# Performance work log

Hardware: AMD Instinct MI355X
Metric: run time of the kernel (lower is better)

The kernel has to match this reference:

```python
import jax, jax.numpy as jnp
import numpy as np

D_INSTR, D_ACT, D_OBJ, TOK = 768, 7, 256, 256


def setup_inputs() -> dict:
    key = jax.random.key(0)
    ks = jax.random.split(key, 10)
    B, NDEMO, NOBJ = 256, 16, 64
    inp = {
        "instr_embedding": jax.random.normal(ks[0], (B, D_INSTR), jnp.float32),
        "demo_object_embeddings": jax.random.normal(ks[1], (NDEMO, B, NOBJ, D_OBJ), jnp.float32),
        "demo_actions": jax.random.normal(ks[2], (NDEMO, B, D_ACT), jnp.float32),
        "current_object_embeddings": jax.random.normal(ks[3], (B, NOBJ, D_OBJ), jnp.float32),
        # learned params (stored as (in, out); equivalent math to torch Linear)
        "W_instr": jax.random.normal(ks[4], (D_INSTR, TOK), jnp.float32) / np.sqrt(D_INSTR),
        "b_instr": jax.random.normal(ks[5], (TOK,), jnp.float32) * 0.01,
        "W_act": jax.random.normal(ks[6], (D_ACT, TOK), jnp.float32) / np.sqrt(D_ACT),
        "b_act": jax.random.normal(ks[7], (TOK,), jnp.float32) * 0.01,
        "W_obj": jax.random.normal(ks[8], (D_OBJ, TOK), jnp.float32) / np.sqrt(D_OBJ),
        "b_obj": jax.random.normal(ks[9], (TOK,), jnp.float32) * 0.01,
    }
    return inp


def reference(instr_embedding, demo_object_embeddings, demo_actions,
              current_object_embeddings, W_instr, b_instr, W_act, b_act,
              W_obj, b_obj):
    # Project everything in single batched GEMMs (structure is uniform across batch,
    # so the per-example Python loop in the original collapses to dense ops).
    instr_tok = instr_embedding @ W_instr + b_instr            # (B, T)
    demo_obj_tok = jnp.einsum('dbnf,ft->dbnt', demo_object_embeddings, W_obj) + b_obj  # (D,B,No,T)
    act_tok = jnp.einsum('dbf,ft->dbt', demo_actions, W_act) + b_act                   # (D,B,T)
    cur_tok = jnp.einsum('bnf,ft->bnt', current_object_embeddings, W_obj) + b_obj      # (B,No,T)

    D, B, No, T = demo_obj_tok.shape
    # Per demo: [objects..., action] -> (D, B, No+1, T), then interleave demos in order.
    demo_block = jnp.concatenate([demo_obj_tok, act_tok[:, :, None, :]], axis=2)
    demo_block = demo_block.transpose(1, 0, 2, 3).reshape(B, D * (No + 1), T)
    # Final sequence: [instr, demo1_objs, demo1_action, ..., current_objs]
    return jnp.concatenate([instr_tok[:, None, :], demo_block, cur_tok], axis=1)
```

## Files before the change

kernel.cpp:

```cpp
#include <hip/hip_runtime.h>
#include <hip/hip_bf16.h>
#include <stdint.h>

#define TOK   256
#define NOBJ  64
#define NDEMO 16
#define BATCH 256
#define SEQ   1105
#define NDG   (NDEMO * BATCH)
#define NGRP  (NDG + BATCH)
#define NHT   (NGRP * 2)
#define NG    4
#define OBJ_BLKS   (NHT / NG)
#define ACT_BLKS   512
#define INSTR_BLKS 128
#define TOTAL_BLKS (ACT_BLKS + INSTR_BLKS + OBJ_BLKS)

typedef __bf16 bf16x8 __attribute__((ext_vector_type(8)));
typedef float  f32x4  __attribute__((ext_vector_type(4)));

static __device__ __forceinline__ unsigned pack_bf16x2(float a, float b) {
    unsigned ua = __float_as_uint(a);
    unsigned ub = __float_as_uint(b);
    unsigned ra = (ua + 0x7FFFu + ((ua >> 16) & 1u)) >> 16;
    unsigned rb = (ub + 0x7FFFu + ((ub >> 16) & 1u)) >> 16;
    return (ra & 0xFFFFu) | (rb << 16);
}

static __device__ __forceinline__ uint16_t f32_to_bf16_bits(float a) {
    unsigned ua = __float_as_uint(a);
    return (uint16_t)((ua + 0x7FFFu + ((ua >> 16) & 1u)) >> 16);
}

static __device__ __forceinline__ bf16x8 pack8(float4 lo, float4 hi) {
    union { uint4 u; bf16x8 b; } r;
    r.u.x = pack_bf16x2(lo.x, lo.y);
    r.u.y = pack_bf16x2(lo.z, lo.w);
    r.u.z = pack_bf16x2(hi.x, hi.y);
    r.u.w = pack_bf16x2(hi.z, hi.w);
    return r.b;
}

static __device__ __forceinline__ void gload_lds16(const float* g, void* l) {
    __builtin_amdgcn_global_load_lds(
        (const __attribute__((address_space(1))) uint32_t*)g,
        (__attribute__((address_space(3))) uint32_t*)l,
        16, 0, 0);
}

__global__ void wconv_frag_kernel(const float* __restrict__ W, uint16_t* __restrict__ Wf) {
    int q = blockIdx.x * 256 + threadIdx.x;
    int lane = q & 63;
    int s  = (q >> 6) & 7;
    int j  = (q >> 9) & 3;
    int wc = (q >> 11) & 3;
    int tcol = wc * 64 + j * 16 + (lane & 15);
    int k0   = s * 32 + (lane >> 4) * 8;
    uint4 w;
    unsigned p[4];
#pragma unroll
    for (int h = 0; h < 4; ++h) {
        float a = W[(size_t)(k0 + 2 * h)     * TOK + tcol];
        float b = W[(size_t)(k0 + 2 * h + 1) * TOK + tcol];
        p[h] = pack_bf16x2(a, b);
    }
    w.x = p[0]; w.y = p[1]; w.z = p[2]; w.w = p[3];
    *reinterpret_cast<uint4*>(Wf + (size_t)q * 8) = w;
}

__global__ __launch_bounds__(256, 2) void fused_kernel(
    const float* __restrict__ demo_obj,
    const float* __restrict__ cur,
    const float* __restrict__ b_obj,
    const __bf16* __restrict__ Wf,
    const float* __restrict__ demo_act,
    const float* __restrict__ W_act,
    const float* __restrict__ b_act,
    const float* __restrict__ instr,
    const float* __restrict__ W_instr,
    const float* __restrict__ b_instr,
    float* __restrict__ out)
{
    __shared__ __align__(16) float lds[2 * 32 * TOK];
    int blk = blockIdx.x;
    int tid = threadIdx.x;

    if (blk >= ACT_BLKS + INSTR_BLKS) {
        int ob = blk - (ACT_BLKS + INSTR_BLKS);
        int h0 = ob * NG;
        const float* base = (h0 < 2 * NDG)
            ? demo_obj + (size_t)h0 * (32 * TOK)
            : cur + (size_t)(h0 - 2 * NDG) * (32 * TOK);

        int wave = tid >> 6, lane = tid & 63;
        int l15 = lane & 15, l4 = lane >> 4;
        int n0 = wave * 64;

        int sr = tid >> 6;
        int sc = tid & 63;
        auto STAGE = [&](int it, int bsel) {
            const float* sb = base + (size_t)it * (32 * TOK);
            float* dst = lds + bsel * (32 * TOK);
#pragma unroll
            for (int i = 0; i < 8; ++i) {
                int r = i * 4 + sr;
                int gch = r * 64 + (sc ^ (r & 7));
                gload_lds16(sb + (size_t)gch * 4, dst + (size_t)(i * 256 + tid) * 4);
            }
        };

        STAGE(0, 0);

        bf16x8 bf[4][8];
        {
            const __bf16* fb = Wf + ((size_t)wave * 32 * 64 + lane) * 8;
#pragma unroll
            for (int j = 0; j < 4; ++j)
#pragma unroll
                for (int s = 0; s < 8; ++s)
                    bf[j][s] = *reinterpret_cast<const bf16x8*>(fb + (size_t)(j * 8 + s) * 64 * 8);
        }

        float bv[4];
#pragma unroll
        for (int j = 0; j < 4; ++j) bv[j] = b_obj[n0 + j * 16 + l15];

#pragma unroll 1
        for (int it = 0; it < NG; ++it) {
            if (it + 1 < NG) {
                STAGE(it + 1, (it + 1) & 1);
                asm volatile("s_waitcnt vmcnt(8)" ::: "memory");
            } else {
                asm volatile("s_waitcnt vmcnt(0)" ::: "memory");
            }
            __builtin_amdgcn_s_barrier();
            __builtin_amdgcn_sched_barrier(0);

            const float* buf = lds + (it & 1) * (32 * TOK);

            f32x4 acc[2][4];
#pragma unroll
            for (int i = 0; i < 2; ++i)
#pragma unroll
                for (int j = 0; j < 4; ++j) {
                    f32x4 z = {0.0f, 0.0f, 0.0f, 0.0f};
                    acc[i][j] = z;
                }

#pragma unroll
            for (int s = 0; s < 8; ++s) {
                bf16x8 a[2];
#pragma unroll
                for (int i = 0; i < 2; ++i) {
                    int r = i * 16 + l15;
                    int c0 = s * 8 + l4 * 2;
                    float4 lo = *reinterpret_cast<const float4*>(buf + r * TOK + ((c0 ^ (r & 7)) * 4));
                    float4 hi = *reinterpret_cast<const float4*>(buf + r * TOK + (((c0 + 1) ^ (r & 7)) * 4));
                    a[i] = pack8(lo, hi);
                }
#pragma unroll
                for (int j = 0; j < 4; ++j) {
                    acc[0][j] = __builtin_amdgcn_mfma_f32_16x16x32_bf16(a[0], bf[j][s], acc[0][j], 0, 0, 0);
                    acc[1][j] = __builtin_amdgcn_mfma_f32_16x16x32_bf16(a[1], bf[j][s], acc[1][j], 0, 0, 0);
                }
            }

            int h = h0 + it;
            int g = h >> 1, half = h & 1;
            int row_base;
            if (h < 2 * NDG) {
                int d = g >> 8, b = g & 255;
                row_base = b * SEQ + 1 + d * (NOBJ + 1) + half * 32;
            } else {
                int b = g - NDG;
                row_base = b * SEQ + 1 + NDEMO * (NOBJ + 1) + half * 32;
            }
#pragma unroll
            for (int i = 0; i < 2; ++i)
#pragma unroll
                for (int j = 0; j < 4; ++j) {
                    int col = n0 + j * 16 + l15;
#pragma unroll
                    for (int r = 0; r < 4; ++r) {
                        int row = row_base + i * 16 + l4 * 4 + r;
                        out[(size_t)row * TOK + col] = acc[i][j][r] + bv[j];
                    }
                }

            __builtin_amdgcn_s_barrier();
        }

    } else if (blk < ACT_BLKS) {
        int g8 = blk * 8;
        int t = tid;
        float v[8];
        float bb = b_act[t];
#pragma unroll
        for (int r = 0; r < 8; ++r) v[r] = bb;
#pragma unroll
        for (int k = 0; k < 7; ++k) {
            float wv = W_act[k * TOK + t];
#pragma unroll
            for (int r = 0; r < 8; ++r)
                v[r] += demo_act[(size_t)(g8 + r) * 7 + k] * wv;
        }
#pragma unroll
        for (int r = 0; r < 8; ++r) {
            int g = g8 + r;
            int d = g >> 8, b = g & 255;
            out[(size_t)(b * SEQ + (d + 1) * (NOBJ + 1)) * TOK + t] = v[r];
        }

    } else {
        int b0 = (blk - ACT_BLKS) * 2;
        int t = tid;
        float* buf = lds;
        const float* src = instr + (size_t)b0 * 768;
#pragma unroll
        for (int i = 0; i < 6; ++i) buf[i * 256 + t] = src[i * 256 + t];
        __syncthreads();
        float a0 = b_instr[t], a1 = a0;
#pragma unroll 4
        for (int k = 0; k < 768; ++k) {
            float wv = W_instr[(size_t)k * TOK + t];
            a0 += buf[k] * wv;
            a1 += buf[768 + k] * wv;
        }
        out[(size_t)b0 * SEQ * TOK + t] = a0;
        out[(size_t)(b0 + 1) * SEQ * TOK + t] = a1;
    }
}

extern "C" void kernel_launch(void* const* d_in, const int* in_sizes, int n_in,
                              void* d_out, int out_size, void* d_ws, size_t ws_size,
                              hipStream_t stream) {
    (void)in_sizes; (void)n_in; (void)out_size; (void)ws_size;
    const float* instr    = (const float*)d_in[0];
    const float* demo_obj = (const float*)d_in[1];
    const float* demo_act = (const float*)d_in[2];
    const float* cur      = (const float*)d_in[3];
    const float* W_instr  = (const float*)d_in[4];
    const float* b_instr  = (const float*)d_in[5];
    const float* W_act    = (const float*)d_in[6];
    const float* b_act    = (const float*)d_in[7];
    const float* W_obj    = (const float*)d_in[8];
    const float* b_obj    = (const float*)d_in[9];
    float* out = (float*)d_out;

    uint16_t* Wf = (uint16_t*)d_ws;

    wconv_frag_kernel<<<32, 256, 0, stream>>>(W_obj, Wf);
    fused_kernel<<<TOTAL_BLKS, 256, 0, stream>>>(
        demo_obj, cur, b_obj, (const __bf16*)d_ws,
        demo_act, W_act, b_act, instr, W_instr, b_instr, out);
}
```

Before: 152.1 us.

## Switch object GEMM to 16-row tiles with triple-buffered LDS prefetch

Each object-projection step now covers 16 rows instead of 32, and each block processes 8 tiles. The LDS pipeline moves from double to triple buffering with a prefetch distance of two, and the barrier at the end of each iteration is dropped. LDS per block shrinks, which lets launch bounds ask for 3 blocks per SM. The aim is to overlap more of the global load latency with compute, at the cost of fewer MFMAs per LDS load and more complex vmcnt bookkeeping.

```diff
diff --git a/kernel.cpp b/kernel.cpp
--- a/kernel.cpp
+++ b/kernel.cpp
@@ -9,9 +9,9 @@
 #define SEQ   1105
 #define NDG   (NDEMO * BATCH)
 #define NGRP  (NDG + BATCH)
-#define NHT   (NGRP * 2)
-#define NG    4
-#define OBJ_BLKS   (NHT / NG)
+#define NQT   (NGRP * 4)
+#define NG    8
+#define OBJ_BLKS   (NQT / NG)
 #define ACT_BLKS   512
 #define INSTR_BLKS 128
 #define TOTAL_BLKS (ACT_BLKS + INSTR_BLKS + OBJ_BLKS)
@@ -68,7 +68,7 @@
     *reinterpret_cast<uint4*>(Wf + (size_t)q * 8) = w;
 }
 
-__global__ __launch_bounds__(256, 2) void fused_kernel(
+__global__ __launch_bounds__(256, 3) void fused_kernel(
     const float* __restrict__ demo_obj,
     const float* __restrict__ cur,
     const float* __restrict__ b_obj,
@@ -81,35 +81,31 @@
     const float* __restrict__ b_instr,
     float* __restrict__ out)
 {
-    __shared__ __align__(16) float lds[2 * 32 * TOK];
+    __shared__ __align__(16) float lds[3 * 16 * TOK];
     int blk = blockIdx.x;
     int tid = threadIdx.x;
 
     if (blk >= ACT_BLKS + INSTR_BLKS) {
         int ob = blk - (ACT_BLKS + INSTR_BLKS);
         int h0 = ob * NG;
-        const float* base = (h0 < 2 * NDG)
-            ? demo_obj + (size_t)h0 * (32 * TOK)
-            : cur + (size_t)(h0 - 2 * NDG) * (32 * TOK);
+        const float* base = (h0 < 4 * NDG)
+            ? demo_obj + (size_t)h0 * (16 * TOK)
+            : cur + (size_t)(h0 - 4 * NDG) * (16 * TOK);
 
         int wave = tid >> 6, lane = tid & 63;
         int l15 = lane & 15, l4 = lane >> 4;
         int n0 = wave * 64;
 
-        int sr = tid >> 6;
-        int sc = tid & 63;
         auto STAGE = [&](int it, int bsel) {
-            const float* sb = base + (size_t)it * (32 * TOK);
-            float* dst = lds + bsel * (32 * TOK);
-#pragma unroll
-            for (int i = 0; i < 8; ++i) {
-                int r = i * 4 + sr;
-                int gch = r * 64 + (sc ^ (r & 7));
+            const float* sb = base + (size_t)it * (16 * TOK);
+            float* dst = lds + bsel * (16 * TOK);
+#pragma unroll
+            for (int i = 0; i < 4; ++i) {
+                int r = i * 4 + wave;
+                int gch = r * 64 + (lane ^ (r & 7));
                 gload_lds16(sb + (size_t)gch * 4, dst + (size_t)(i * 256 + tid) * 4);
             }
         };
-
-        STAGE(0, 0);
 
         bf16x8 bf[4][8];
         {
@@ -120,74 +116,74 @@
                 for (int s = 0; s < 8; ++s)
                     bf[j][s] = *reinterpret_cast<const bf16x8*>(fb + (size_t)(j * 8 + s) * 64 * 8);
         }
+#pragma unroll
+        for (int j = 0; j < 4; ++j)
+#pragma unroll
+            for (int s = 0; s < 8; ++s)
+                asm volatile("" : "+v"(bf[j][s]));
 
         float bv[4];
 #pragma unroll
         for (int j = 0; j < 4; ++j) bv[j] = b_obj[n0 + j * 16 + l15];
 
+        STAGE(0, 0);
+        STAGE(1, 1);
+
+        int bc = 0;
 #pragma unroll 1
         for (int it = 0; it < NG; ++it) {
-            if (it + 1 < NG) {
-                STAGE(it + 1, (it + 1) & 1);
-                asm volatile("s_waitcnt vmcnt(8)" ::: "memory");
-            } else {
-                asm volatile("s_waitcnt vmcnt(0)" ::: "memory");
-            }
+            if (it == 0)           asm volatile("s_waitcnt vmcnt(4)"  ::: "memory");
+            else if (it == NG - 1) asm volatile("s_waitcnt vmcnt(16)" ::: "memory");
+            else                   asm volatile("s_waitcnt vmcnt(20)" ::: "memory");
             __builtin_amdgcn_s_barrier();
             __builtin_amdgcn_sched_barrier(0);
 
-            const float* buf = lds + (it & 1) * (32 * TOK);
-
-            f32x4 acc[2][4];
-#pragma unroll
-            for (int i = 0; i < 2; ++i)
-#pragma unroll
-                for (int j = 0; j < 4; ++j) {
-                    f32x4 z = {0.0f, 0.0f, 0.0f, 0.0f};
-                    acc[i][j] = z;
-                }
+            if (it + 2 < NG) {
+                int bs = bc >= 1 ? bc - 1 : bc + 2;
+                STAGE(it + 2, bs);
+            }
+
+            const float* buf = lds + bc * (16 * TOK);
+
+            f32x4 acc[4];
+#pragma unroll
+            for (int j = 0; j < 4; ++j) {
+                f32x4 z = {0.0f, 0.0f, 0.0f, 0.0f};
+                acc[j] = z;
+            }
 
 #pragma unroll
             for (int s = 0; s < 8; ++s) {
-                bf16x8 a[2];
-#pragma unroll
-                for (int i = 0; i < 2; ++i) {
-                    int r = i * 16 + l15;
-                    int c0 = s * 8 + l4 * 2;
-                    float4 lo = *reinterpret_cast<const float4*>(buf + r * TOK + ((c0 ^ (r & 7)) * 4));
-                    float4 hi = *reinterpret_cast<const float4*>(buf + r * TOK + (((c0 + 1) ^ (r & 7)) * 4));
-                    a[i] = pack8(lo, hi);
-                }
-#pragma unroll
-                for (int j = 0; j < 4; ++j) {
-                    acc[0][j] = __builtin_amdgcn_mfma_f32_16x16x32_bf16(a[0], bf[j][s], acc[0][j], 0, 0, 0);
-                    acc[1][j] = __builtin_amdgcn_mfma_f32_16x16x32_bf16(a[1], bf[j][s], acc[1][j], 0, 0, 0);
-                }
+                int c0 = s * 8 + l4 * 2;
+                float4 lo = *reinterpret_cast<const float4*>(buf + l15 * TOK + ((c0 ^ (l15 & 7)) * 4));
+                float4 hi = *reinterpret_cast<const float4*>(buf + l15 * TOK + (((c0 + 1) ^ (l15 & 7)) * 4));
+                bf16x8 a = pack8(lo, hi);
+#pragma unroll
+                for (int j = 0; j < 4; ++j)
+                    acc[j] = __builtin_amdgcn_mfma_f32_16x16x32_bf16(a, bf[j][s], acc[j], 0, 0, 0);
             }
 
             int h = h0 + it;
-            int g = h >> 1, half = h & 1;
+            int g = h >> 2, q = h & 3;
             int row_base;
-            if (h < 2 * NDG) {
+            if (h < 4 * NDG) {
                 int d = g >> 8, b = g & 255;
-                row_base = b * SEQ + 1 + d * (NOBJ + 1) + half * 32;
+                row_base = b * SEQ + 1 + d * (NOBJ + 1) + q * 16;
             } else {
                 int b = g - NDG;
-                row_base = b * SEQ + 1 + NDEMO * (NOBJ + 1) + half * 32;
-            }
-#pragma unroll
-            for (int i = 0; i < 2; ++i)
-#pragma unroll
-                for (int j = 0; j < 4; ++j) {
-                    int col = n0 + j * 16 + l15;
-#pragma unroll
-                    for (int r = 0; r < 4; ++r) {
-                        int row = row_base + i * 16 + l4 * 4 + r;
-                        out[(size_t)row * TOK + col] = acc[i][j][r] + bv[j];
-                    }
+                row_base = b * SEQ + 1 + NDEMO * (NOBJ + 1) + q * 16;
+            }
+#pragma unroll
+            for (int j = 0; j < 4; ++j) {
+                int col = n0 + j * 16 + l15;
+#pragma unroll
+                for (int r = 0; r < 4; ++r) {
+                    int row = row_base + l4 * 4 + r;
+                    out[(size_t)row * TOK + col] = acc[j][r] + bv[j];
                 }
-
-            __builtin_amdgcn_s_barrier();
+            }
+
+            bc = bc == 2 ? 0 : bc + 1;
         }
 
     } else if (blk < ACT_BLKS) {
```

Measured after the change: 240.8 us. +58.3%, slower.
